# Kernel optimization log

Hardware: AMD Instinct MI355X
Metric: run time of the kernel (lower is better)

The kernel has to match this reference:

```python
import jax, jax.numpy as jnp
import numpy as np

B, V, H, CIN, S = 32, 32, 32, 256, 256


def setup_inputs() -> dict:
    key = jax.random.key(0)
    k1, k2 = jax.random.split(key)
    x = jax.random.normal(k1, (B, V, H, CIN), dtype=jnp.float32)  # log-prob inputs
    # accumulators are positive (Constant(1) init in original); use uniform in (0.1, 1.1)
    accumulators = jax.random.uniform(k2, (V, H, CIN, S), dtype=jnp.float32,
                                      minval=0.1, maxval=1.1)
    return {"x": x, "accumulators": accumulators}


def reference(x, accumulators):
    # log_softmax of log(accumulators) over the input-channel axis (axis=2)
    log_w = jax.nn.log_softmax(jnp.log(accumulators), axis=2)  # (V,H,CIN,S)
    # scopes-first layout: (V,H,B,CIN)
    xs = jnp.transpose(x, (1, 2, 0, 3))
    # stable logmatmul: out[v,h,b,s] = logsumexp_k( xs[v,h,b,k] + log_w[v,h,k,s] )
    x_max = jnp.max(xs, axis=-1, keepdims=True)          # (V,H,B,1)
    w_max = jnp.max(log_w, axis=2, keepdims=True)        # (V,H,1,S)
    prod = jnp.einsum('vhbk,vhks->vhbs',
                      jnp.exp(xs - x_max), jnp.exp(log_w - w_max))
    out_scopes_first = jnp.log(prod) + x_max + w_max     # (V,H,B,S)
    return jnp.transpose(out_scopes_first, (2, 0, 1, 3))  # (B,V,H,S)
```

## Files before the change

### kernel.cpp

```cpp
#include <hip/hip_runtime.h>

#define NV 32
#define NH 32
#define NB 32
#define NK 256
#define NS 256

__device__ __forceinline__ void async_load16(const float* g, float* l) {
    __builtin_amdgcn_global_load_lds(
        (const __attribute__((address_space(1))) void*)g,
        (__attribute__((address_space(3))) void*)l,
        16, 0, 0);
}

__global__ __launch_bounds__(256, 2)
void slsum_kernel(const float* __restrict__ x,
                  const float* __restrict__ acc,
                  float* __restrict__ out)
{
    __shared__ float E[NB][NK];
    __shared__ float As[32][NS];
    __shared__ float xmaxS[NB];

    const int tid  = threadIdx.x;
    const int lane = tid & 63;
    const int wv   = tid >> 6;
    const int vh   = blockIdx.x;

    const float* xp = x   + (size_t)vh * NK;
    const float* ap = acc + (size_t)vh * (NK * NS);
    float*       op = out + (size_t)vh * NS;

    float4* Asf4 = reinterpret_cast<float4*>(&As[0][0]);
    float4* Ef4  = reinterpret_cast<float4*>(&E[0][0]);

    #pragma unroll
    for (int i = 0; i < 8; ++i) {
        int idx = i * 256 + tid;
        int b = idx >> 6, c4 = idx & 63;
        Asf4[idx] = *reinterpret_cast<const float4*>(xp + (size_t)b * (NV*NH*NK) + c4 * 4);
    }
    __syncthreads();

    {
        const int r = tid >> 3, sub = tid & 7;
        float m = -3.402823466e38f;
        #pragma unroll
        for (int j = 0; j < 8; ++j) {
            float4 f = Asf4[r * 64 + sub * 8 + j];
            m = fmaxf(m, fmaxf(fmaxf(f.x, f.y), fmaxf(f.z, f.w)));
        }
        m = fmaxf(m, __shfl_xor(m, 1));
        m = fmaxf(m, __shfl_xor(m, 2));
        m = fmaxf(m, __shfl_xor(m, 4));
        if (sub == 0) xmaxS[r] = m;
    }
    __syncthreads();

    #pragma unroll
    for (int i = 0; i < 8; ++i) {
        int idx = i * 256 + tid;
        int b = idx >> 6;
        const float xm = xmaxS[b];
        float4 f = Asf4[idx];
        Ef4[idx] = make_float4(__expf(f.x - xm), __expf(f.y - xm),
                               __expf(f.z - xm), __expf(f.w - xm));
    }

    const int brow = wv;
    const int scol = lane;

    float4 accv[8];
    #pragma unroll
    for (int i = 0; i < 8; ++i) accv[i] = make_float4(0.f, 0.f, 0.f, 0.f);
    float4 asumv = make_float4(0.f, 0.f, 0.f, 0.f);

    for (int ch = 0; ch < 8; ++ch) {
        __syncthreads();
        #pragma unroll
        for (int j = 0; j < 8; ++j) {
            const int row = wv * 8 + j;
            async_load16(ap + (size_t)(ch * 32 + row) * NS + lane * 4, &As[row][0]);
        }
        __syncthreads();

        #pragma unroll
        for (int k4 = 0; k4 < 8; ++k4) {
            const float4 a0 = Asf4[(k4*4+0)*64 + scol];
            const float4 a1 = Asf4[(k4*4+1)*64 + scol];
            const float4 a2 = Asf4[(k4*4+2)*64 + scol];
            const float4 a3 = Asf4[(k4*4+3)*64 + scol];
            asumv.x += (a0.x + a1.x) + (a2.x + a3.x);
            asumv.y += (a0.y + a1.y) + (a2.y + a3.y);
            asumv.z += (a0.z + a1.z) + (a2.z + a3.z);
            asumv.w += (a0.w + a1.w) + (a2.w + a3.w);
            #pragma unroll
            for (int i = 0; i < 8; ++i) {
                const float4 e = Ef4[(brow*8 + i)*64 + ch*8 + k4];
                accv[i].x = fmaf(e.x, a0.x, fmaf(e.y, a1.x, fmaf(e.z, a2.x, fmaf(e.w, a3.x, accv[i].x))));
                accv[i].y = fmaf(e.x, a0.y, fmaf(e.y, a1.y, fmaf(e.z, a2.y, fmaf(e.w, a3.y, accv[i].y))));
                accv[i].z = fmaf(e.x, a0.z, fmaf(e.y, a1.z, fmaf(e.z, a2.z, fmaf(e.w, a3.z, accv[i].z))));
                accv[i].w = fmaf(e.x, a0.w, fmaf(e.y, a1.w, fmaf(e.z, a2.w, fmaf(e.w, a3.w, accv[i].w))));
            }
        }
    }

    const float la0 = __logf(asumv.x);
    const float la1 = __logf(asumv.y);
    const float la2 = __logf(asumv.z);
    const float la3 = __logf(asumv.w);

    #pragma unroll
    for (int i = 0; i < 8; ++i) {
        const int b = brow * 8 + i;
        const float xm = xmaxS[b];
        float4 o;
        o.x = __logf(accv[i].x) + xm - la0;
        o.y = __logf(accv[i].y) + xm - la1;
        o.z = __logf(accv[i].z) + xm - la2;
        o.w = __logf(accv[i].w) + xm - la3;
        *reinterpret_cast<float4*>(op + (size_t)b * (NV*NH*NS) + scol * 4) = o;
    }
}

extern "C" void kernel_launch(void* const* d_in, const int* in_sizes, int n_in,
                              void* d_out, int out_size, void* d_ws, size_t ws_size,
                              hipStream_t stream) {
    const float* x   = (const float*)d_in[0];
    const float* acc = (const float*)d_in[1];
    float* out = (float*)d_out;
    slsum_kernel<<<dim3(NV * NH), dim3(256), 0, stream>>>(x, acc, out);
}
```

Before: 425.9 us.

## Double-buffer accumulator chunks with async LDS loads to overlap with FMA

Replaces the single 32-row accumulator staging buffer with two 16-row LDS buffers. The next chunk is prefetched via global_load_lds while the current chunk is being consumed. The first chunk's load is issued before the x tile is loaded, and the x tile now stages directly in the E buffer. This hides global-memory latency behind compute and keeps the same total LDS footprint, at the cost of twice as many barrier iterations.

```diff
diff --git a/kernel.cpp b/kernel.cpp
--- a/kernel.cpp
+++ b/kernel.cpp
@@ -5,6 +5,8 @@
 #define NB 32
 #define NK 256
 #define NS 256
+#define CH_ROWS 16
+#define NCH (NK / CH_ROWS)
 
 __device__ __forceinline__ void async_load16(const float* g, float* l) {
     __builtin_amdgcn_global_load_lds(
@@ -19,7 +21,7 @@
                   float* __restrict__ out)
 {
     __shared__ float E[NB][NK];
-    __shared__ float As[32][NS];
+    __shared__ float Abuf[2][CH_ROWS][NS];
     __shared__ float xmaxS[NB];
 
     const int tid  = threadIdx.x;
@@ -31,14 +33,19 @@
     const float* ap = acc + (size_t)vh * (NK * NS);
     float*       op = out + (size_t)vh * NS;
 
-    float4* Asf4 = reinterpret_cast<float4*>(&As[0][0]);
-    float4* Ef4  = reinterpret_cast<float4*>(&E[0][0]);
+    float4* Ef4 = reinterpret_cast<float4*>(&E[0][0]);
+
+    #pragma unroll
+    for (int j = 0; j < 4; ++j) {
+        const int row = wv * 4 + j;
+        async_load16(ap + (size_t)row * NS + lane * 4, &Abuf[0][row][0]);
+    }
 
     #pragma unroll
     for (int i = 0; i < 8; ++i) {
         int idx = i * 256 + tid;
         int b = idx >> 6, c4 = idx & 63;
-        Asf4[idx] = *reinterpret_cast<const float4*>(xp + (size_t)b * (NV*NH*NK) + c4 * 4);
+        Ef4[idx] = *reinterpret_cast<const float4*>(xp + (size_t)b * (NV*NH*NK) + c4 * 4);
     }
     __syncthreads();
 
@@ -47,7 +54,7 @@
         float m = -3.402823466e38f;
         #pragma unroll
         for (int j = 0; j < 8; ++j) {
-            float4 f = Asf4[r * 64 + sub * 8 + j];
+            float4 f = Ef4[r * 64 + sub * 8 + j];
             m = fmaxf(m, fmaxf(fmaxf(f.x, f.y), fmaxf(f.z, f.w)));
         }
         m = fmaxf(m, __shfl_xor(m, 1));
@@ -62,7 +69,7 @@
         int idx = i * 256 + tid;
         int b = idx >> 6;
         const float xm = xmaxS[b];
-        float4 f = Asf4[idx];
+        float4 f = Ef4[idx];
         Ef4[idx] = make_float4(__expf(f.x - xm), __expf(f.y - xm),
                                __expf(f.z - xm), __expf(f.w - xm));
     }
@@ -75,28 +82,33 @@
     for (int i = 0; i < 8; ++i) accv[i] = make_float4(0.f, 0.f, 0.f, 0.f);
     float4 asumv = make_float4(0.f, 0.f, 0.f, 0.f);
 
-    for (int ch = 0; ch < 8; ++ch) {
-        __syncthreads();
-        #pragma unroll
-        for (int j = 0; j < 8; ++j) {
-            const int row = wv * 8 + j;
-            async_load16(ap + (size_t)(ch * 32 + row) * NS + lane * 4, &As[row][0]);
-        }
+    for (int ch = 0; ch < NCH; ++ch) {
+        const int cur = ch & 1;
         __syncthreads();
 
+        if (ch + 1 < NCH) {
+            #pragma unroll
+            for (int j = 0; j < 4; ++j) {
+                const int row = wv * 4 + j;
+                async_load16(ap + (size_t)((ch + 1) * CH_ROWS + row) * NS + lane * 4,
+                             &Abuf[cur ^ 1][row][0]);
+            }
+        }
+
+        const float4* buff4 = reinterpret_cast<const float4*>(&Abuf[cur][0][0]);
         #pragma unroll
-        for (int k4 = 0; k4 < 8; ++k4) {
-            const float4 a0 = Asf4[(k4*4+0)*64 + scol];
-            const float4 a1 = Asf4[(k4*4+1)*64 + scol];
-            const float4 a2 = Asf4[(k4*4+2)*64 + scol];
-            const float4 a3 = Asf4[(k4*4+3)*64 + scol];
+        for (int k4 = 0; k4 < CH_ROWS / 4; ++k4) {
+            const float4 a0 = buff4[(k4*4+0)*64 + scol];
+            const float4 a1 = buff4[(k4*4+1)*64 + scol];
+            const float4 a2 = buff4[(k4*4+2)*64 + scol];
+            const float4 a3 = buff4[(k4*4+3)*64 + scol];
             asumv.x += (a0.x + a1.x) + (a2.x + a3.x);
             asumv.y += (a0.y + a1.y) + (a2.y + a3.y);
             asumv.z += (a0.z + a1.z) + (a2.z + a3.z);
             asumv.w += (a0.w + a1.w) + (a2.w + a3.w);
             #pragma unroll
             for (int i = 0; i < 8; ++i) {
-                const float4 e = Ef4[(brow*8 + i)*64 + ch*8 + k4];
+                const float4 e = Ef4[(brow*8 + i)*64 + ch*4 + k4];
                 accv[i].x = fmaf(e.x, a0.x, fmaf(e.y, a1.x, fmaf(e.z, a2.x, fmaf(e.w, a3.x, accv[i].x))));
                 accv[i].y = fmaf(e.x, a0.y, fmaf(e.y, a1.y, fmaf(e.z, a2.y, fmaf(e.w, a3.y, accv[i].y))));
                 accv[i].z = fmaf(e.x, a0.z, fmaf(e.y, a1.z, fmaf(e.z, a2.z, fmaf(e.w, a3.z, accv[i].z))));
```

Measured after the change: 391.7 us. 1.09x faster.

## Replace LDS staging of accumulators with register double-buffered direct global loads

Applied to the files above, without the earlier changes.

Removes the LDS tile for accumulators and the per-chunk barriers. Each wave now loads its accumulator rows straight into registers with a two-group software prefetch that overlaps the FMA work. The E tile reuses LDS for the raw x values, and the launch-bounds occupancy hint is raised to 3. The trade-off is that all four waves redundantly fetch the same accumulator data from global memory and rely on cache hits, and register pressure rises.

```diff
diff --git a/kernel.cpp b/kernel.cpp
--- a/kernel.cpp
+++ b/kernel.cpp
@@ -5,21 +5,38 @@
 #define NB 32
 #define NK 256
 #define NS 256
+#define NG (NK / 4)
 
-__device__ __forceinline__ void async_load16(const float* g, float* l) {
-    __builtin_amdgcn_global_load_lds(
-        (const __attribute__((address_space(1))) void*)g,
-        (__attribute__((address_space(3))) void*)l,
-        16, 0, 0);
+__device__ __forceinline__ void ld_group(float4 (&buf)[4], const float* base, int g) {
+    #pragma unroll
+    for (int j = 0; j < 4; ++j)
+        buf[j] = *reinterpret_cast<const float4*>(base + (size_t)(g * 4 + j) * NS);
 }
 
-__global__ __launch_bounds__(256, 2)
+__device__ __forceinline__ void compute_group(int g, const float4 (&buf)[4],
+                                              const float4* Ef4, int erow0,
+                                              float4 (&accv)[8], float4& asum) {
+    const float4 a0 = buf[0], a1 = buf[1], a2 = buf[2], a3 = buf[3];
+    asum.x += (a0.x + a1.x) + (a2.x + a3.x);
+    asum.y += (a0.y + a1.y) + (a2.y + a3.y);
+    asum.z += (a0.z + a1.z) + (a2.z + a3.z);
+    asum.w += (a0.w + a1.w) + (a2.w + a3.w);
+    #pragma unroll
+    for (int i = 0; i < 8; ++i) {
+        const float4 e = Ef4[(erow0 + i) * 64 + g];
+        accv[i].x = fmaf(e.x, a0.x, fmaf(e.y, a1.x, fmaf(e.z, a2.x, fmaf(e.w, a3.x, accv[i].x))));
+        accv[i].y = fmaf(e.x, a0.y, fmaf(e.y, a1.y, fmaf(e.z, a2.y, fmaf(e.w, a3.y, accv[i].y))));
+        accv[i].z = fmaf(e.x, a0.z, fmaf(e.y, a1.z, fmaf(e.z, a2.z, fmaf(e.w, a3.z, accv[i].z))));
+        accv[i].w = fmaf(e.x, a0.w, fmaf(e.y, a1.w, fmaf(e.z, a2.w, fmaf(e.w, a3.w, accv[i].w))));
+    }
+}
+
+__global__ __launch_bounds__(256, 3)
 void slsum_kernel(const float* __restrict__ x,
                   const float* __restrict__ acc,
                   float* __restrict__ out)
 {
     __shared__ float E[NB][NK];
-    __shared__ float As[32][NS];
     __shared__ float xmaxS[NB];
 
     const int tid  = threadIdx.x;
@@ -28,17 +45,20 @@
     const int vh   = blockIdx.x;
 
     const float* xp = x   + (size_t)vh * NK;
-    const float* ap = acc + (size_t)vh * (NK * NS);
+    const float* ap = acc + (size_t)vh * (NK * NS) + lane * 4;
     float*       op = out + (size_t)vh * NS;
 
-    float4* Asf4 = reinterpret_cast<float4*>(&As[0][0]);
-    float4* Ef4  = reinterpret_cast<float4*>(&E[0][0]);
+    float4* Ef4 = reinterpret_cast<float4*>(&E[0][0]);
+
+    float4 bufA[4], bufB[4];
+    ld_group(bufA, ap, 0);
+    ld_group(bufB, ap, 1);
 
     #pragma unroll
     for (int i = 0; i < 8; ++i) {
         int idx = i * 256 + tid;
         int b = idx >> 6, c4 = idx & 63;
-        Asf4[idx] = *reinterpret_cast<const float4*>(xp + (size_t)b * (NV*NH*NK) + c4 * 4);
+        Ef4[idx] = *reinterpret_cast<const float4*>(xp + (size_t)b * (NV*NH*NK) + c4 * 4);
     }
     __syncthreads();
 
@@ -47,7 +67,7 @@
         float m = -3.402823466e38f;
         #pragma unroll
         for (int j = 0; j < 8; ++j) {
-            float4 f = Asf4[r * 64 + sub * 8 + j];
+            float4 f = Ef4[r * 64 + sub * 8 + j];
             m = fmaxf(m, fmaxf(fmaxf(f.x, f.y), fmaxf(f.z, f.w)));
         }
         m = fmaxf(m, __shfl_xor(m, 1));
@@ -62,48 +82,27 @@
         int idx = i * 256 + tid;
         int b = idx >> 6;
         const float xm = xmaxS[b];
-        float4 f = Asf4[idx];
+        float4 f = Ef4[idx];
         Ef4[idx] = make_float4(__expf(f.x - xm), __expf(f.y - xm),
                                __expf(f.z - xm), __expf(f.w - xm));
     }
+    __syncthreads();
 
-    const int brow = wv;
-    const int scol = lane;
+    const int erow0 = wv * 8;
 
     float4 accv[8];
     #pragma unroll
     for (int i = 0; i < 8; ++i) accv[i] = make_float4(0.f, 0.f, 0.f, 0.f);
     float4 asumv = make_float4(0.f, 0.f, 0.f, 0.f);
 
-    for (int ch = 0; ch < 8; ++ch) {
-        __syncthreads();
-        #pragma unroll
-        for (int j = 0; j < 8; ++j) {
-            const int row = wv * 8 + j;
-            async_load16(ap + (size_t)(ch * 32 + row) * NS + lane * 4, &As[row][0]);
-        }
-        __syncthreads();
-
-        #pragma unroll
-        for (int k4 = 0; k4 < 8; ++k4) {
-            const float4 a0 = Asf4[(k4*4+0)*64 + scol];
-            const float4 a1 = Asf4[(k4*4+1)*64 + scol];
-            const float4 a2 = Asf4[(k4*4+2)*64 + scol];
-            const float4 a3 = Asf4[(k4*4+3)*64 + scol];
-            asumv.x += (a0.x + a1.x) + (a2.x + a3.x);
-            asumv.y += (a0.y + a1.y) + (a2.y + a3.y);
-            asumv.z += (a0.z + a1.z) + (a2.z + a3.z);
-            asumv.w += (a0.w + a1.w) + (a2.w + a3.w);
-            #pragma unroll
-            for (int i = 0; i < 8; ++i) {
-                const float4 e = Ef4[(brow*8 + i)*64 + ch*8 + k4];
-                accv[i].x = fmaf(e.x, a0.x, fmaf(e.y, a1.x, fmaf(e.z, a2.x, fmaf(e.w, a3.x, accv[i].x))));
-                accv[i].y = fmaf(e.x, a0.y, fmaf(e.y, a1.y, fmaf(e.z, a2.y, fmaf(e.w, a3.y, accv[i].y))));
-                accv[i].z = fmaf(e.x, a0.z, fmaf(e.y, a1.z, fmaf(e.z, a2.z, fmaf(e.w, a3.z, accv[i].z))));
-                accv[i].w = fmaf(e.x, a0.w, fmaf(e.y, a1.w, fmaf(e.z, a2.w, fmaf(e.w, a3.w, accv[i].w))));
-            }
-        }
+    for (int g = 0; g < NG - 2; g += 2) {
+        compute_group(g,     bufA, Ef4, erow0, accv, asumv);
+        ld_group(bufA, ap, g + 2);
+        compute_group(g + 1, bufB, Ef4, erow0, accv, asumv);
+        ld_group(bufB, ap, g + 3);
     }
+    compute_group(NG - 2, bufA, Ef4, erow0, accv, asumv);
+    compute_group(NG - 1, bufB, Ef4, erow0, accv, asumv);
 
     const float la0 = __logf(asumv.x);
     const float la1 = __logf(asumv.y);
@@ -112,14 +111,14 @@
 
     #pragma unroll
     for (int i = 0; i < 8; ++i) {
-        const int b = brow * 8 + i;
+        const int b = erow0 + i;
         const float xm = xmaxS[b];
         float4 o;
         o.x = __logf(accv[i].x) + xm - la0;
         o.y = __logf(accv[i].y) + xm - la1;
         o.z = __logf(accv[i].z) + xm - la2;
         o.w = __logf(accv[i].w) + xm - la3;
-        *reinterpret_cast<float4*>(op + (size_t)b * (NV*NH*NS) + scol * 4) = o;
+        *reinterpret_cast<float4*>(op + (size_t)b * (NV*NH*NS) + lane * 4) = o;
     }
 }
 
```

Measured after the change: 398.8 us. 1.07x faster.
